# Performance work log

Hardware: AMD Instinct MI355X
Metric: run time of the kernel (lower is better)

The kernel has to match this reference:

```python
import jax, jax.numpy as jnp
import numpy as np

B, QN, KVN = 4, 512, 512
QD, KD, H, VD = 512, 512, 256, 256


def setup_inputs() -> dict:
    key = jax.random.key(0)
    ks = jax.random.split(key, 6)
    q = jax.random.normal(ks[0], (B, QN, QD), dtype=jnp.float32)
    k = jax.random.normal(ks[1], (B, KVN, KD), dtype=jnp.float32)
    v = jax.random.normal(ks[2], (B, KVN, VD), dtype=jnp.float32)
    # Linear weights (torch nn.Linear stores [out, in]; bias=False)
    Wq = jax.random.normal(ks[3], (H, QD), dtype=jnp.float32) / np.sqrt(QD)
    Wk = jax.random.normal(ks[4], (H, KD), dtype=jnp.float32) / np.sqrt(KD)
    wv = jax.random.normal(ks[5], (H,), dtype=jnp.float32) / np.sqrt(H)
    return {"q": q, "k": k, "v": v, "Wq": Wq, "Wk": Wk, "wv": wv}


def reference(q, k, v, Wq, Wk, wv):
    # Project queries and keys to hidden dim H
    qh = jnp.einsum("bqd,hd->bqh", q, Wq)  # [B, QN, H]
    kh = jnp.einsum("bkd,hd->bkh", k, Wk)  # [B, KVN, H]
    # Broadcast add + tanh: [B, QN, KVN, H]
    energy = jnp.tanh(qh[:, :, None, :] + kh[:, None, :, :])
    # Score projection to scalar per (q, kv) pair
    scores = jnp.einsum("bqkh,h->bqk", energy, wv)  # [B, QN, KVN]
    attention = jax.nn.softmax(scores, axis=-1)
    # Dropout omitted (inference mode)
    output = jnp.einsum("bqk,bkv->bqv", attention, v)  # [B, QN, VD]
    return (output, attention)
```

## Files before the change

kernel.cpp:

```cpp
#include <hip/hip_runtime.h>

#define B_ 4
#define QN 512
#define KVN 512
#define QD_ 512
#define H_ 256
#define VD_ 256
#define TOTR 2048

typedef __attribute__((ext_vector_type(8))) short bf16x8;
typedef __attribute__((ext_vector_type(4))) float f32x4;
typedef __attribute__((ext_vector_type(4))) unsigned short u16x4;
typedef unsigned short u16;

__device__ __forceinline__ float rcp_(float x) { return __builtin_amdgcn_rcpf(x); }
__device__ __forceinline__ float ex2_(float x) { return __builtin_amdgcn_exp2f(x); }

__device__ __forceinline__ u16 bf16_rne(float x) {
    unsigned u = __float_as_uint(x);
    unsigned r = u + 0x7FFFu + ((u >> 16) & 1u);
    return (u16)(r >> 16);
}
__device__ __forceinline__ void split2(float x, u16& h, u16& l) {
    h = bf16_rne(x);
    float hf = __uint_as_float((unsigned)h << 16);
    l = bf16_rne(x - hf);
}
__device__ __forceinline__ void split4(float4 a, u16x4& h, u16x4& l) {
    u16 hh, ll;
    split2(a.x, hh, ll); h[0] = hh; l[0] = ll;
    split2(a.y, hh, ll); h[1] = hh; l[1] = ll;
    split2(a.z, hh, ll); h[2] = hh; l[2] = ll;
    split2(a.w, hh, ll); h[3] = hh; l[3] = ll;
}

__global__ __launch_bounds__(256) void prep(const float* __restrict__ q,
                                            const float* __restrict__ k,
                                            const float* __restrict__ Wq,
                                            const float* __restrict__ Wk,
                                            const float* __restrict__ v,
                                            u16* __restrict__ q_hi, u16* __restrict__ q_lo,
                                            u16* __restrict__ k_hi, u16* __restrict__ k_lo,
                                            u16* __restrict__ w_hi, u16* __restrict__ w_lo,
                                            u16* __restrict__ vt_hi, u16* __restrict__ vt_lo) {
    __shared__ float ts[64][65];
    const int tid = threadIdx.x;
    if (blockIdx.x < 2304) {
        const int NQ = 2048 * 512 / 4, NW = 256 * 512 / 4;
        int idx = blockIdx.x * 256 + tid;
        const float* src; u16 *dh, *dl; int off;
        if (idx < NQ)               { src = q;  dh = q_hi; dl = q_lo; off = idx; }
        else if (idx < 2 * NQ)      { src = k;  dh = k_hi; dl = k_lo; off = idx - NQ; }
        else if (idx < 2 * NQ + NW) { src = Wq; dh = w_hi; dl = w_lo; off = idx - 2 * NQ; }
        else { src = Wk; dh = w_hi + 256 * 512; dl = w_lo + 256 * 512; off = idx - 2 * NQ - NW; }
        float4 v4 = ((const float4*)src)[off];
        u16x4 h, l;
        split4(v4, h, l);
        *(u16x4*)(dh + off * 4) = h;
        *(u16x4*)(dl + off * 4) = l;
    } else {
        int bid = blockIdx.x - 2304;
        int j0 = (bid & 7) * 64, n0 = ((bid >> 3) & 3) * 64, b = bid >> 5;
#pragma unroll
        for (int t = 0; t < 4; ++t) {
            int idx = t * 256 + tid;
            int j = idx >> 4, nq = idx & 15;
            float4 v4 = *(const float4*)(v + ((size_t)b * KVN + j0 + j) * VD_ + n0 + nq * 4);
            *(float4*)&ts[j][nq * 4] = v4;
        }
        __syncthreads();
#pragma unroll
        for (int t = 0; t < 4; ++t) {
            int idx = t * 256 + tid;
            int jq = idx & 15, n = idx >> 4;
            u16x4 h, l;
            u16 hh, ll;
#pragma unroll
            for (int e = 0; e < 4; ++e) {
                split2(ts[jq * 4 + e][n], hh, ll);
                h[e] = hh; l[e] = ll;
            }
            size_t off = ((size_t)b * VD_ + n0 + n) * KVN + j0 + jq * 4;
            *(u16x4*)(vt_hi + off) = h;
            *(u16x4*)(vt_lo + off) = l;
        }
    }
}

__global__ __launch_bounds__(256) void proj_mfma(const u16* __restrict__ q_hi, const u16* __restrict__ q_lo,
                                                 const u16* __restrict__ k_hi, const u16* __restrict__ k_lo,
                                                 const u16* __restrict__ w_hi, const u16* __restrict__ w_lo,
                                                 const float* __restrict__ wv,
                                                 float* __restrict__ eqw, float* __restrict__ ekT) {
    const int z = blockIdx.z;
    const u16* __restrict__ Ah_g = z ? k_hi : q_hi;
    const u16* __restrict__ Al_g = z ? k_lo : q_lo;
    const u16* __restrict__ Bh_g = w_hi + (size_t)z * H_ * QD_;
    const u16* __restrict__ Bl_g = w_lo + (size_t)z * H_ * QD_;
    __shared__ u16 Ash[4][32][8], Asl[4][32][8], Bsh[4][32][8], Bsl[4][32][8];
    const int tid = threadIdx.x;
    const int wave = tid >> 6, lane = tid & 63;
    const int fl = lane & 15, kg = lane >> 4;
    const int r0 = blockIdx.y * 32, c0 = blockIdx.x * 32;
    const int ar = 16 * (wave & 1), bc = 16 * (wave >> 1);
    const int frow = (tid & 127) >> 2, fkq = tid & 3, fsel = tid >> 7;
    f32x4 acc = {};
    for (int k0 = 0; k0 < QD_; k0 += 32) {
        __syncthreads();
        {
            const u16* as = (fsel ? Al_g : Ah_g) + (size_t)(r0 + frow) * QD_ + k0 + fkq * 8;
            u16* ad = fsel ? &Asl[fkq][frow][0] : &Ash[fkq][frow][0];
            *(uint4*)ad = *(const uint4*)as;
            const u16* bs = (fsel ? Bl_g : Bh_g) + (size_t)(c0 + frow) * QD_ + k0 + fkq * 8;
            u16* bd = fsel ? &Bsl[fkq][frow][0] : &Bsh[fkq][frow][0];
            *(uint4*)bd = *(const uint4*)bs;
        }
        __syncthreads();
        bf16x8 a_h = *(const bf16x8*)&Ash[kg][ar + fl][0];
        bf16x8 a_l = *(const bf16x8*)&Asl[kg][ar + fl][0];
        bf16x8 b_h = *(const bf16x8*)&Bsh[kg][bc + fl][0];
        bf16x8 b_l = *(const bf16x8*)&Bsl[kg][bc + fl][0];
        acc = __builtin_amdgcn_mfma_f32_16x16x32_bf16(a_h, b_h, acc, 0, 0, 0);
        acc = __builtin_amdgcn_mfma_f32_16x16x32_bf16(a_h, b_l, acc, 0, 0, 0);
        acc = __builtin_amdgcn_mfma_f32_16x16x32_bf16(a_l, b_h, acc, 0, 0, 0);
    }
    const float cs = 2.8853900817779268f;
    const int rg = kg * 4;
    if (z == 1) {
        float4 o = {ex2_(acc[0] * cs), ex2_(acc[1] * cs), ex2_(acc[2] * cs), ex2_(acc[3] * cs)};
        *(float4*)(ekT + (size_t)(c0 + bc + fl) * TOTR + r0 + ar + rg) = o;
    } else {
        float iw = rcp_(wv[c0 + bc + fl]);
#pragma unroll
        for (int r = 0; r < 4; ++r)
            eqw[(size_t)(r0 + ar + rg + r) * H_ + c0 + bc + fl] = ex2_(acc[r] * cs) * iw;
    }
}

__global__ __launch_bounds__(256, 4) void scores_v7(const float* __restrict__ eqw,
                                                    const float* __restrict__ ekT,
                                                    const float* __restrict__ wv,
                                                    float* __restrict__ scpart) {
    const int tid = threadIdx.x;
    const int wid = tid >> 6, lane = tid & 63;
    const int hs = blockIdx.z;
    const int h0 = hs * 32;
    const int row0 = blockIdx.y * 16;
    const int b = row0 >> 9;
    const int jloc = blockIdx.x * 256 + wid * 64 + lane;
    const int colg = b * KVN + jloc;

    float ekr[32], iwv[32];
#pragma unroll
    for (int hh = 0; hh < 32; ++hh)
        ekr[hh] = ekT[(size_t)(h0 + hh) * TOTR + colg];
#pragma unroll
    for (int g = 0; g < 8; ++g) {
        float4 w4 = *(const float4*)(wv + h0 + 4 * g);
        iwv[4 * g + 0] = rcp_(w4.x);
        iwv[4 * g + 1] = rcp_(w4.y);
        iwv[4 * g + 2] = rcp_(w4.z);
        iwv[4 * g + 3] = rcp_(w4.w);
    }

    const float* __restrict__ eqrow = eqw + (size_t)row0 * H_ + h0;
    float* __restrict__ outp = scpart + (size_t)hs * TOTR * KVN + (size_t)row0 * KVN + jloc;

#pragma unroll 2
    for (int qq = 0; qq < 16; ++qq) {
        const float* ep = eqrow + (size_t)qq * H_;
        float s = 0.f;
#pragma unroll
        for (int g = 0; g < 8; ++g) {
            float4 e = *(const float4*)(ep + 4 * g);
            float d0 = __builtin_fmaf(ekr[4 * g + 0], e.x, iwv[4 * g + 0]);
            float d1 = __builtin_fmaf(ekr[4 * g + 1], e.y, iwv[4 * g + 1]);
            float d2 = __builtin_fmaf(ekr[4 * g + 2], e.z, iwv[4 * g + 2]);
            float d3 = __builtin_fmaf(ekr[4 * g + 3], e.w, iwv[4 * g + 3]);
            s = __builtin_fmaf(d0 + d1, rcp_(d0 * d1), s);
            s = __builtin_fmaf(d2 + d3, rcp_(d2 * d3), s);
        }
        outp[(size_t)qq * KVN] = s;
    }
}

__global__ __launch_bounds__(256) void softmax2(const float* __restrict__ scpart,
                                                float* __restrict__ attn,
                                                u16* __restrict__ at_hi,
                                                u16* __restrict__ at_lo) {
    const size_t PS = (size_t)TOTR * KVN;
    int row = blockIdx.x;
    int tid = threadIdx.x;
    const float* p = scpart + (size_t)row * KVN;
    float x0 = 0.f, x1 = 0.f;
#pragma unroll
    for (int hsplit = 0; hsplit < 8; ++hsplit) {
        x0 += p[hsplit * PS + tid];
        x1 += p[hsplit * PS + tid + 256];
    }
    float e0 = __expf(-2.0f * x0), e1 = __expf(-2.0f * x1);
    float s = e0 + e1;
#pragma unroll
    for (int d = 1; d < 64; d <<= 1) s += __shfl_xor(s, d);
    __shared__ float reds[4];
    int wave = tid >> 6, lane = tid & 63;
    if (lane == 0) reds[wave] = s;
    __syncthreads();
    s = reds[0] + reds[1] + reds[2] + reds[3];
    float inv = rcp_(s);
    float r0v = e0 * inv, r1v = e1 * inv;
    float* o = attn + (size_t)row * KVN;
    o[tid] = r0v;
    o[tid + 256] = r1v;
    u16 h, l;
    size_t base = (size_t)row * KVN;
    split2(r0v, h, l);
    at_hi[base + tid] = h; at_lo[base + tid] = l;
    split2(r1v, h, l);
    at_hi[base + tid + 256] = h; at_lo[base + tid + 256] = l;
}

__global__ __launch_bounds__(256) void out_mfma(const u16* __restrict__ vt_hi, const u16* __restrict__ vt_lo,
                                                const u16* __restrict__ at_hi, const u16* __restrict__ at_lo,
                                                float* __restrict__ out) {
    const int b = blockIdx.z;
    const u16* __restrict__ Ah_g = vt_hi + (size_t)b * VD_ * KVN;
    const u16* __restrict__ Al_g = vt_lo + (size_t)b * VD_ * KVN;
    const u16* __restrict__ Bh_g = at_hi + (size_t)b * QN * KVN;
    const u16* __restrict__ Bl_g = at_lo + (size_t)b * QN * KVN;
    float* __restrict__ outb = out + (size_t)b * QN * VD_;
    __shared__ u16 Ash[4][32][8], Asl[4][32][8], Bsh[4][32][8], Bsl[4][32][8];
    const int tid = threadIdx.x;
    const int wave = tid >> 6, lane = tid & 63;
    const int fl = lane & 15, kg = lane >> 4;
    const int r0 = blockIdx.y * 32;
    const int c0 = blockIdx.x * 32;
    const int ar = 16 * (wave & 1), bc = 16 * (wave >> 1);
    const int frow = (tid & 127) >> 2, fkq = tid & 3, fsel = tid >> 7;
    f32x4 acc = {};
    for (int k0 = 0; k0 < KVN; k0 += 32) {
        __syncthreads();
        {
            const u16* as = (fsel ? Al_g : Ah_g) + (size_t)(r0 + frow) * KVN + k0 + fkq * 8;
            u16* ad = fsel ? &Asl[fkq][frow][0] : &Ash[fkq][frow][0];
            *(uint4*)ad = *(const uint4*)as;
            const u16* bs = (fsel ? Bl_g : Bh_g) + (size_t)(c0 + frow) * KVN + k0 + fkq * 8;
            u16* bd = fsel ? &Bsl[fkq][frow][0] : &Bsh[fkq][frow][0];
            *(uint4*)bd = *(const uint4*)bs;
        }
        __syncthreads();
        bf16x8 a_h = *(const bf16x8*)&Ash[kg][ar + fl][0];
        bf16x8 a_l = *(const bf16x8*)&Asl[kg][ar + fl][0];
        bf16x8 b_h = *(const bf16x8*)&Bsh[kg][bc + fl][0];
        bf16x8 b_l = *(const bf16x8*)&Bsl[kg][bc + fl][0];
        acc = __builtin_amdgcn_mfma_f32_16x16x32_bf16(a_h, b_h, acc, 0, 0, 0);
        acc = __builtin_amdgcn_mfma_f32_16x16x32_bf16(a_h, b_l, acc, 0, 0, 0);
        acc = __builtin_amdgcn_mfma_f32_16x16x32_bf16(a_l, b_h, acc, 0, 0, 0);
    }
    const int rg = kg * 4;
    float4 o = {acc[0], acc[1], acc[2], acc[3]};
    *(float4*)(outb + (size_t)(c0 + bc + fl) * VD_ + r0 + ar + rg) = o;
}

extern "C" void kernel_launch(void* const* d_in, const int* in_sizes, int n_in,
                              void* d_out, int out_size, void* d_ws, size_t ws_size,
                              hipStream_t stream) {
    const float* q  = (const float*)d_in[0];
    const float* k  = (const float*)d_in[1];
    const float* v  = (const float*)d_in[2];
    const float* Wq = (const float*)d_in[3];
    const float* Wk = (const float*)d_in[4];
    const float* wv = (const float*)d_in[5];
    float* out  = (float*)d_out;
    float* attn = out + (size_t)B_ * QN * VD_;

    float* eqw = (float*)d_ws;
    float* ekT = eqw + (size_t)TOTR * H_;
    u16* q_hi = (u16*)(ekT + (size_t)H_ * TOTR);
    u16* q_lo = q_hi + 2048 * 512;
    u16* k_hi = q_lo + 2048 * 512;
    u16* k_lo = k_hi + 2048 * 512;
    u16* w_hi = k_lo + 2048 * 512;
    u16* w_lo = w_hi + 512 * 512;
    u16* vt_hi = w_lo + 512 * 512;
    u16* vt_lo = vt_hi + (size_t)B_ * VD_ * KVN;
    float* scpart = (float*)(vt_lo + (size_t)B_ * VD_ * KVN);
    u16* at_hi = q_hi;
    u16* at_lo = q_lo;

    prep<<<2432, 256, 0, stream>>>(q, k, Wq, Wk, v, q_hi, q_lo, k_hi, k_lo,
                                   w_hi, w_lo, vt_hi, vt_lo);
    proj_mfma<<<dim3(H_ / 32, 2048 / 32, 2), 256, 0, stream>>>(q_hi, q_lo, k_hi, k_lo,
                                                               w_hi, w_lo, wv, eqw, ekT);
    scores_v7<<<dim3(2, TOTR / 16, 8), 256, 0, stream>>>(eqw, ekT, wv, scpart);
    softmax2<<<TOTR, 256, 0, stream>>>(scpart, attn, at_hi, at_lo);
    out_mfma<<<dim3(QN / 32, VD_ / 32, B_), 256, 0, stream>>>(vt_hi, vt_lo, at_hi, at_lo, out);
}
```

Baseline: 74.43 us.

## Fuse score computation with softmax and reduce reciprocals per four-term group

Merges the score kernel and the softmax kernel into one. Each 512-thread block now loops over the full hidden dimension for 4 query rows and does the row softmax in-block, so the 8-way partial-score buffer is no longer written and read back through global memory. It also combines four tanh-style terms into a single reciprocal through a shared-denominator identity, and precomputes 1/wv once in the prep kernel. In exchange there are fewer blocks (512), a longer serial loop per thread, ekT reloaded for every 4 rows, and possible precision or overflow risk from multiplying four denominators together.

Measured after the change: 74.90 us. No clear change (+0.6%).

```diff
diff --git a/kernel.cpp b/kernel.cpp
--- a/kernel.cpp
+++ b/kernel.cpp
@@ -39,10 +39,12 @@
                                             const float* __restrict__ Wq,
                                             const float* __restrict__ Wk,
                                             const float* __restrict__ v,
+                                            const float* __restrict__ wv,
                                             u16* __restrict__ q_hi, u16* __restrict__ q_lo,
                                             u16* __restrict__ k_hi, u16* __restrict__ k_lo,
                                             u16* __restrict__ w_hi, u16* __restrict__ w_lo,
-                                            u16* __restrict__ vt_hi, u16* __restrict__ vt_lo) {
+                                            u16* __restrict__ vt_hi, u16* __restrict__ vt_lo,
+                                            float* __restrict__ iwg) {
     __shared__ float ts[64][65];
     const int tid = threadIdx.x;
     if (blockIdx.x < 2304) {
@@ -58,7 +60,7 @@
         split4(v4, h, l);
         *(u16x4*)(dh + off * 4) = h;
         *(u16x4*)(dl + off * 4) = l;
-    } else {
+    } else if (blockIdx.x < 2432) {
         int bid = blockIdx.x - 2304;
         int j0 = (bid & 7) * 64, n0 = ((bid >> 3) & 3) * 64, b = bid >> 5;
 #pragma unroll
@@ -84,13 +86,15 @@
             *(u16x4*)(vt_hi + off) = h;
             *(u16x4*)(vt_lo + off) = l;
         }
+    } else {
+        iwg[tid] = rcp_(wv[tid]);
     }
 }
 
 __global__ __launch_bounds__(256) void proj_mfma(const u16* __restrict__ q_hi, const u16* __restrict__ q_lo,
                                                  const u16* __restrict__ k_hi, const u16* __restrict__ k_lo,
                                                  const u16* __restrict__ w_hi, const u16* __restrict__ w_lo,
-                                                 const float* __restrict__ wv,
+                                                 const float* __restrict__ iwg,
                                                  float* __restrict__ eqw, float* __restrict__ ekT) {
     const int z = blockIdx.z;
     const u16* __restrict__ Ah_g = z ? k_hi : q_hi;
@@ -130,94 +134,78 @@
         float4 o = {ex2_(acc[0] * cs), ex2_(acc[1] * cs), ex2_(acc[2] * cs), ex2_(acc[3] * cs)};
         *(float4*)(ekT + (size_t)(c0 + bc + fl) * TOTR + r0 + ar + rg) = o;
     } else {
-        float iw = rcp_(wv[c0 + bc + fl]);
+        float iw = iwg[c0 + bc + fl];
 #pragma unroll
         for (int r = 0; r < 4; ++r)
             eqw[(size_t)(r0 + ar + rg + r) * H_ + c0 + bc + fl] = ex2_(acc[r] * cs) * iw;
     }
 }
 
-__global__ __launch_bounds__(256, 4) void scores_v7(const float* __restrict__ eqw,
+__global__ __launch_bounds__(512, 4) void scores_sm(const float* __restrict__ eqw,
                                                     const float* __restrict__ ekT,
-                                                    const float* __restrict__ wv,
-                                                    float* __restrict__ scpart) {
-    const int tid = threadIdx.x;
+                                                    const float* __restrict__ iwg,
+                                                    float* __restrict__ attn,
+                                                    u16* __restrict__ at_hi,
+                                                    u16* __restrict__ at_lo) {
+    const int tid = threadIdx.x;
+    const int row0 = blockIdx.x * 4;
+    const int b = row0 >> 9;
+    const int colg = b * KVN + tid;
+    float sc[4] = {};
+#pragma unroll 2
+    for (int ch = 0; ch < 16; ++ch) {
+        const int h0 = ch * 16;
+        float ekr[16];
+#pragma unroll
+        for (int t = 0; t < 16; ++t)
+            ekr[t] = ekT[(size_t)(h0 + t) * TOTR + colg];
+        float4 iw4[4];
+#pragma unroll
+        for (int g = 0; g < 4; ++g) iw4[g] = *(const float4*)(iwg + h0 + 4 * g);
+#pragma unroll
+        for (int qq = 0; qq < 4; ++qq) {
+            const float* ep = eqw + (size_t)(row0 + qq) * H_ + h0;
+            float s = 0.f;
+#pragma unroll
+            for (int g = 0; g < 4; ++g) {
+                float4 e = *(const float4*)(ep + 4 * g);
+                float d0 = __builtin_fmaf(ekr[4 * g + 0], e.x, iw4[g].x);
+                float d1 = __builtin_fmaf(ekr[4 * g + 1], e.y, iw4[g].y);
+                float d2 = __builtin_fmaf(ekr[4 * g + 2], e.z, iw4[g].z);
+                float d3 = __builtin_fmaf(ekr[4 * g + 3], e.w, iw4[g].w);
+                float ab = d0 * d1, cd = d2 * d3;
+                float num = __builtin_fmaf(d0 + d1, cd, (d2 + d3) * ab);
+                s = __builtin_fmaf(num, rcp_(ab * cd), s);
+            }
+            sc[qq] += s;
+        }
+    }
+    __shared__ float red[8][4];
     const int wid = tid >> 6, lane = tid & 63;
-    const int hs = blockIdx.z;
-    const int h0 = hs * 32;
-    const int row0 = blockIdx.y * 16;
-    const int b = row0 >> 9;
-    const int jloc = blockIdx.x * 256 + wid * 64 + lane;
-    const int colg = b * KVN + jloc;
-
-    float ekr[32], iwv[32];
-#pragma unroll
-    for (int hh = 0; hh < 32; ++hh)
-        ekr[hh] = ekT[(size_t)(h0 + hh) * TOTR + colg];
-#pragma unroll
-    for (int g = 0; g < 8; ++g) {
-        float4 w4 = *(const float4*)(wv + h0 + 4 * g);
-        iwv[4 * g + 0] = rcp_(w4.x);
-        iwv[4 * g + 1] = rcp_(w4.y);
-        iwv[4 * g + 2] = rcp_(w4.z);
-        iwv[4 * g + 3] = rcp_(w4.w);
-    }
-
-    const float* __restrict__ eqrow = eqw + (size_t)row0 * H_ + h0;
-    float* __restrict__ outp = scpart + (size_t)hs * TOTR * KVN + (size_t)row0 * KVN + jloc;
-
-#pragma unroll 2
-    for (int qq = 0; qq < 16; ++qq) {
-        const float* ep = eqrow + (size_t)qq * H_;
-        float s = 0.f;
-#pragma unroll
-        for (int g = 0; g < 8; ++g) {
-            float4 e = *(const float4*)(ep + 4 * g);
-            float d0 = __builtin_fmaf(ekr[4 * g + 0], e.x, iwv[4 * g + 0]);
-            float d1 = __builtin_fmaf(ekr[4 * g + 1], e.y, iwv[4 * g + 1]);
-            float d2 = __builtin_fmaf(ekr[4 * g + 2], e.z, iwv[4 * g + 2]);
-            float d3 = __builtin_fmaf(ekr[4 * g + 3], e.w, iwv[4 * g + 3]);
-            s = __builtin_fmaf(d0 + d1, rcp_(d0 * d1), s);
-            s = __builtin_fmaf(d2 + d3, rcp_(d2 * d3), s);
-        }
-        outp[(size_t)qq * KVN] = s;
-    }
-}
-
-__global__ __launch_bounds__(256) void softmax2(const float* __restrict__ scpart,
-                                                float* __restrict__ attn,
-                                                u16* __restrict__ at_hi,
-                                                u16* __restrict__ at_lo) {
-    const size_t PS = (size_t)TOTR * KVN;
-    int row = blockIdx.x;
-    int tid = threadIdx.x;
-    const float* p = scpart + (size_t)row * KVN;
-    float x0 = 0.f, x1 = 0.f;
-#pragma unroll
-    for (int hsplit = 0; hsplit < 8; ++hsplit) {
-        x0 += p[hsplit * PS + tid];
-        x1 += p[hsplit * PS + tid + 256];
-    }
-    float e0 = __expf(-2.0f * x0), e1 = __expf(-2.0f * x1);
-    float s = e0 + e1;
-#pragma unroll
-    for (int d = 1; d < 64; d <<= 1) s += __shfl_xor(s, d);
-    __shared__ float reds[4];
-    int wave = tid >> 6, lane = tid & 63;
-    if (lane == 0) reds[wave] = s;
+    float ev[4];
+#pragma unroll
+    for (int qq = 0; qq < 4; ++qq)
+        ev[qq] = ex2_(sc[qq] * -2.8853900817779268f);
+#pragma unroll
+    for (int qq = 0; qq < 4; ++qq) {
+        float ssum = ev[qq];
+#pragma unroll
+        for (int d = 1; d < 64; d <<= 1) ssum += __shfl_xor(ssum, d);
+        if (lane == 0) red[wid][qq] = ssum;
+    }
     __syncthreads();
-    s = reds[0] + reds[1] + reds[2] + reds[3];
-    float inv = rcp_(s);
-    float r0v = e0 * inv, r1v = e1 * inv;
-    float* o = attn + (size_t)row * KVN;
-    o[tid] = r0v;
-    o[tid + 256] = r1v;
-    u16 h, l;
-    size_t base = (size_t)row * KVN;
-    split2(r0v, h, l);
-    at_hi[base + tid] = h; at_lo[base + tid] = l;
-    split2(r1v, h, l);
-    at_hi[base + tid + 256] = h; at_lo[base + tid + 256] = l;
+#pragma unroll
+    for (int qq = 0; qq < 4; ++qq) {
+        float tot = ((red[0][qq] + red[1][qq]) + (red[2][qq] + red[3][qq])) +
+                    ((red[4][qq] + red[5][qq]) + (red[6][qq] + red[7][qq]));
+        float a = ev[qq] * rcp_(tot);
+        size_t base = (size_t)(row0 + qq) * KVN + tid;
+        attn[base] = a;
+        u16 h, l;
+        split2(a, h, l);
+        at_hi[base] = h;
+        at_lo[base] = l;
+    }
 }
 
 __global__ __launch_bounds__(256) void out_mfma(const u16* __restrict__ vt_hi, const u16* __restrict__ vt_lo,
@@ -276,7 +264,8 @@
 
     float* eqw = (float*)d_ws;
     float* ekT = eqw + (size_t)TOTR * H_;
-    u16* q_hi = (u16*)(ekT + (size_t)H_ * TOTR);
+    float* iwg = ekT + (size_t)H_ * TOTR;
+    u16* q_hi = (u16*)(iwg + 256);
     u16* q_lo = q_hi + 2048 * 512;
     u16* k_hi = q_lo + 2048 * 512;
     u16* k_lo = k_hi + 2048 * 512;
@@ -284,15 +273,13 @@
     u16* w_lo = w_hi + 512 * 512;
     u16* vt_hi = w_lo + 512 * 512;
     u16* vt_lo = vt_hi + (size_t)B_ * VD_ * KVN;
-    float* scpart = (float*)(vt_lo + (size_t)B_ * VD_ * KVN);
     u16* at_hi = q_hi;
     u16* at_lo = q_lo;
 
-    prep<<<2432, 256, 0, stream>>>(q, k, Wq, Wk, v, q_hi, q_lo, k_hi, k_lo,
-                                   w_hi, w_lo, vt_hi, vt_lo);
+    prep<<<2433, 256, 0, stream>>>(q, k, Wq, Wk, v, wv, q_hi, q_lo, k_hi, k_lo,
+                                   w_hi, w_lo, vt_hi, vt_lo, iwg);
     proj_mfma<<<dim3(H_ / 32, 2048 / 32, 2), 256, 0, stream>>>(q_hi, q_lo, k_hi, k_lo,
-                                                               w_hi, w_lo, wv, eqw, ekT);
-    scores_v7<<<dim3(2, TOTR / 16, 8), 256, 0, stream>>>(eqw, ekT, wv, scpart);
-    softmax2<<<TOTR, 256, 0, stream>>>(scpart, attn, at_hi, at_lo);
+                                                               w_hi, w_lo, iwg, eqw, ekT);
+    scores_sm<<<TOTR / 4, 512, 0, stream>>>(eqw, ekT, iwg, attn, at_hi, at_lo);
     out_mfma<<<dim3(QN / 32, VD_ / 32, B_), 256, 0, stream>>>(vt_hi, vt_lo, at_hi, at_lo, out);
 }
```
